# Kernel optimization log

Hardware: AMD Instinct MI355X
Metric: run time of the kernel (lower is better)

The kernel has to match this reference:

```python
import jax, jax.numpy as jnp
import numpy as np
import math

N, N_OBS, D, H, P = 500000, 200000, 32, 128, 4


def setup_inputs() -> dict:
    key = jax.random.key(0)
    ks = jax.random.split(key, 10)
    h = jax.random.normal(ks[0], (N, H), dtype=jnp.float32)
    p = jax.random.normal(ks[1], (N, 2 * D), dtype=jnp.float32)
    X_obs = jax.random.normal(ks[2], (N_OBS, D), dtype=jnp.float32)
    M_obs = (jax.random.uniform(ks[3], (N_OBS, D)) > 0.5).astype(jnp.float32)
    # unique sorted indices into [0, N) so the scatter-update is well defined
    i_obs = jnp.sort(jax.random.permutation(ks[4], N)[:N_OBS]).astype(jnp.int32)
    std = math.sqrt(2.0 / (4 + P))
    w_prep = std * jax.random.normal(ks[5], (D, 4, P), dtype=jnp.float32)
    bias_prep = 0.1 + jnp.zeros((D, P), dtype=jnp.float32)
    k = 1.0 / math.sqrt(H)
    W_ih = jax.random.uniform(ks[6], (3 * H, P * D), minval=-k, maxval=k, dtype=jnp.float32)
    W_hh = jax.random.uniform(ks[7], (3 * H, H), minval=-k, maxval=k, dtype=jnp.float32)
    b_ih = jax.random.uniform(ks[8], (3 * H,), minval=-k, maxval=k, dtype=jnp.float32)
    b_hh = jax.random.uniform(ks[9], (3 * H,), minval=-k, maxval=k, dtype=jnp.float32)
    return {"h": h, "p": p, "X_obs": X_obs, "M_obs": M_obs, "i_obs": i_obs,
            "w_prep": w_prep, "bias_prep": bias_prep,
            "W_ih": W_ih, "W_hh": W_hh, "b_ih": b_ih, "b_hh": b_hh}


def gru_cell(x, h, W_ih, W_hh, b_ih, b_hh):
    # torch.nn.GRUCell semantics; gate order r, z, n
    gi = x @ W_ih.T + b_ih            # [n, 3H]
    gh = h @ W_hh.T + b_hh            # [n, 3H]
    i_r, i_z, i_n = jnp.split(gi, 3, axis=1)
    h_r, h_z, h_n = jnp.split(gh, 3, axis=1)
    r = jax.nn.sigmoid(i_r + h_r)
    z = jax.nn.sigmoid(i_z + h_z)
    n = jnp.tanh(i_n + r * h_n)
    return (1.0 - z) * n + z * h


def reference(h, p, X_obs, M_obs, i_obs, w_prep, bias_prep, W_ih, W_hh, b_ih, b_hh):
    p_obs = p[i_obs]                                     # gather [n_obs, 2D]
    mean, logvar = jnp.split(p_obs, 2, axis=1)
    lv = jnp.clip(logvar, -10.0, 10.0)
    sigma = jnp.clip(jnp.exp(0.5 * lv), 1e-6, 1e6)
    error = jnp.clip((X_obs - mean) / sigma, -1e6, 1e6)
    log_lik_c = float(np.log(np.sqrt(2 * np.pi)))
    losses = 0.5 * ((error ** 2 + lv + 2.0 * log_lik_c) * M_obs)  # [n_obs, D]
    feats = jnp.stack([X_obs, mean, lv, error], axis=2)  # [n_obs, D, 4]
    gi = jnp.einsum('ndk,dkp->ndp', feats, w_prep) + bias_prep  # per-channel small matmul
    gi = jax.nn.relu(gi) * M_obs[..., None]              # mask broadcast over prep_hidden
    gru_in = gi.reshape(gi.shape[0], D * P)              # [n_obs, D*P], D-major like torch view
    h_obs = h[i_obs]
    h_new = gru_cell(gru_in, h_obs, W_ih, W_hh, b_ih, b_hh)
    h = h.at[i_obs].set(h_new)                           # scatter update
    return (h, losses)
```

## Files before the change

kernel.cpp:

```cpp
#include <hip/hip_runtime.h>


typedef __attribute__((ext_vector_type(8))) short bf16x8;
typedef __attribute__((ext_vector_type(4))) float f32x4;

__device__ inline unsigned short f2bf_rne(float x) {
    union { float f; unsigned int u; } v; v.f = x;
    unsigned int r = (v.u + 0x7fffu + ((v.u >> 16) & 1u)) >> 16;
    return (unsigned short)r;
}
__device__ inline unsigned short f2bf_tr(float x) {
    return (unsigned short)(__float_as_uint(x) >> 16);
}
__device__ inline float bf2f(unsigned short u) {
    return __uint_as_float(((unsigned int)u) << 16);
}
__device__ inline float fast_sigmoid(float x) {
    return __builtin_amdgcn_rcpf(1.f + __expf(-x));
}
__device__ inline float fast_tanh(float x) {
    const float a = fabsf(x);
    const float t = __expf(-2.f * a);
    const float r = (1.f - t) * __builtin_amdgcn_rcpf(1.f + t);
    return __builtin_copysignf(r, x);
}
__device__ inline void gl_lds16(const float* g, float* lds_base) {
    __builtin_amdgcn_global_load_lds(
        (const __attribute__((address_space(1))) void*)g,
        (__attribute__((address_space(3))) void*)lds_base, 16, 0, 0);
}

__global__ __launch_bounds__(256) void k_prepack(const float* __restrict__ W_ih,
                                                 const float* __restrict__ W_hh,
                                                 unsigned short* __restrict__ B) {
    const int i = blockIdx.x * 256 + threadIdx.x;
    const int w    = i / 12288;
    const int rem  = i - w * 12288;
    const int f    = rem >> 9;
    const int rem2 = rem & 511;
    const int l    = rem2 >> 3;
    const int j    = rem2 & 7;
    const int c    = w * 16 + (l & 15);
    const int ko   = (l >> 4) * 8 + j;
    float val;
    if (f < 8) {
        const int k = f * 32 + ko;
        val = (k < 128) ? W_ih[c * 128 + k] : W_hh[c * 128 + (k - 128)];
    } else if (f < 16) {
        const int k = (f - 8) * 32 + ko;
        val = (k < 128) ? W_ih[(128 + c) * 128 + k] : W_hh[(128 + c) * 128 + (k - 128)];
    } else if (f < 20) {
        const int k = (f - 16) * 32 + ko;
        val = W_ih[(256 + c) * 128 + k];
    } else {
        const int k = (f - 20 + 4) * 32 + ko;
        val = W_hh[(256 + c) * 128 + (k - 128)];
    }
    B[i] = f2bf_rne(val);
}

__global__ __launch_bounds__(256) void k_flag(const int* __restrict__ i_obs,
                                              unsigned char* __restrict__ flags, int n) {
    const int i = blockIdx.x * 256 + threadIdx.x;
    if (i < n) flags[i_obs[i]] = 1;
}

__global__ __launch_bounds__(256) void k_copy(const f32x4* __restrict__ src,
                                              f32x4* __restrict__ dst, long n4) {
    long i = (long)blockIdx.x * blockDim.x + threadIdx.x;
    long stride = (long)gridDim.x * blockDim.x;
    for (; i < n4; i += stride) dst[i] = src[i];
}

struct PrefRegs {
    float mean[4], lv[4], X[4], M[4];
    f32x4 hv[4];
    int idx[4];
};

__global__ __launch_bounds__(512) void k_pers(
    const float* __restrict__ h, const float* __restrict__ p,
    const float* __restrict__ X_obs, const float* __restrict__ M_obs,
    const int* __restrict__ i_obs,
    const float* __restrict__ w_prep, const float* __restrict__ bias_prep,
    const unsigned short* __restrict__ Bpk,
    const float* __restrict__ b_ih, const float* __restrict__ b_hh,
    float* __restrict__ out_h, float* __restrict__ out_losses,
    const unsigned char* __restrict__ flags,
    int NT, int chunk, int Nh, int do_copy)
{
    __shared__ unsigned short sA[4 * 8 * 64 * 8];
    __shared__ float hcopy[160 * 128];
    __shared__ int sIdx[64];

    const int tid  = threadIdx.x;
    const int d    = tid & 31;
    const int wid  = tid >> 6;
    const int lane = tid & 63;
    const int cw   = wid * 16 + (lane & 15);

    float wp[16], bp[4];
    #pragma unroll
    for (int t = 0; t < 16; ++t) wp[t] = w_prep[d * 16 + t];
    #pragma unroll
    for (int t = 0; t < 4; ++t) bp[t] = bias_prep[d * 4 + t];

    bf16x8 breg[24];
    {
        const bf16x8* bsrc = reinterpret_cast<const bf16x8*>(Bpk) + wid * 1536;
        #pragma unroll
        for (int f = 0; f < 24; ++f) breg[f] = bsrc[f * 64 + lane];
    }
    const float bR  = b_ih[cw]       + b_hh[cw];
    const float bZ  = b_ih[128 + cw] + b_hh[128 + cw];
    const float bIN = b_ih[256 + cw];
    const float bHN = b_hh[256 + cw];

    const int ksA  = d >> 3;
    const int l16  = ((d >> 1) & 3) * 16;
    const int j0   = (d & 1) * 4;
    const int ksE  = 4 + (cw >> 5);
    const int l16E = ((cw >> 3) & 3) * 16;
    const int jE   = cw & 7;

    const bf16x8* aptr = reinterpret_cast<const bf16x8*>(sA);

    PrefRegs R;

    auto G_load = [&](int t) {
        const int row0 = t * 64;
        #pragma unroll
        for (int ps = 0; ps < 4; ++ps) {
            const int r   = ps * 16 + (tid >> 5);
            const int idx = i_obs[row0 + r];
            R.idx[ps]  = idx;
            R.mean[ps] = p[(size_t)idx * 64 + d];
            R.lv[ps]   = p[(size_t)idx * 64 + 32 + d];
            R.X[ps]    = X_obs[(size_t)(row0 + r) * 32 + d];
            R.M[ps]    = M_obs[(size_t)(row0 + r) * 32 + d];
            R.hv[ps]   = *reinterpret_cast<const f32x4*>(h + (size_t)idx * 128 + d * 4);
        }
    };

    auto COPY_issue = [&](int t) {
        const long rlo = (long)t * chunk;
        const float* hs = h + rlo * 128;
        const int rbase = wid * 20;
        #pragma unroll
        for (int q = 0; q < 10; ++q) {
            const int row = rbase + q * 2;
            gl_lds16(hs + (size_t)row * 128 + lane * 4, &hcopy[row * 128]);
        }
    };

    auto COPY_store = [&](int t) {
        const long rlo = (long)t * chunk;
        f32x4* hd = reinterpret_cast<f32x4*>(out_h + rlo * 128);
        const unsigned char* fl = flags + rlo;
        const f32x4* hc = reinterpret_cast<const f32x4*>(hcopy);
        #pragma unroll
        for (int ii = 0; ii < 10; ++ii) {
            const int i5 = ii * 512 + tid;
            if (!fl[i5 >> 5]) __builtin_nontemporal_store(hc[i5], &hd[i5]);
        }
    };

    auto C_phase = [&](int t) {
        const int row0 = t * 64;
        #pragma unroll
        for (int ps = 0; ps < 4; ++ps) {
            const int r  = ps * 16 + (tid >> 5);
            const int mt = r >> 4;
            if (d == 0) sIdx[r] = R.idx[ps];
            const float lv      = fminf(fmaxf(R.lv[ps], -10.f), 10.f);
            const float inv_sig = __expf(-0.5f * lv);
            const float X = R.X[ps], Mv = R.M[ps], mean = R.mean[ps];
            const float err = fminf(fmaxf((X - mean) * inv_sig, -1e6f), 1e6f);
            out_losses[(size_t)(row0 + r) * 32 + d] =
                0.5f * ((err * err + lv + 1.8378770664093453f) * Mv);
            ushort4 u;
            float g0 = fmaf(X, wp[0], fmaf(mean, wp[4], fmaf(lv, wp[8],  fmaf(err, wp[12], bp[0]))));
            float g1 = fmaf(X, wp[1], fmaf(mean, wp[5], fmaf(lv, wp[9],  fmaf(err, wp[13], bp[1]))));
            float g2 = fmaf(X, wp[2], fmaf(mean, wp[6], fmaf(lv, wp[10], fmaf(err, wp[14], bp[2]))));
            float g3 = fmaf(X, wp[3], fmaf(mean, wp[7], fmaf(lv, wp[11], fmaf(err, wp[15], bp[3]))));
            u.x = f2bf_tr(fmaxf(g0, 0.f) * Mv);
            u.y = f2bf_tr(fmaxf(g1, 0.f) * Mv);
            u.z = f2bf_tr(fmaxf(g2, 0.f) * Mv);
            u.w = f2bf_tr(fmaxf(g3, 0.f) * Mv);
            *reinterpret_cast<ushort4*>(&sA[((mt * 8 + ksA) * 64 + (r & 15) + l16) * 8 + j0]) = u;
            const f32x4 v = R.hv[ps];
            ushort4 uh;
            uh.x = f2bf_tr(v.x); uh.y = f2bf_tr(v.y); uh.z = f2bf_tr(v.z); uh.w = f2bf_tr(v.w);
            *reinterpret_cast<ushort4*>(&sA[((mt * 8 + ksA + 4) * 64 + (r & 15) + l16) * 8 + j0]) = uh;
        }
    };

    auto M_phase = [&]() {
        #pragma unroll
        for (int mt = 0; mt < 4; ++mt) {
            f32x4 accR = {0.f, 0.f, 0.f, 0.f};
            f32x4 accZ = {0.f, 0.f, 0.f, 0.f};
            f32x4 accIN = {0.f, 0.f, 0.f, 0.f};
            f32x4 accHN = {0.f, 0.f, 0.f, 0.f};
            #pragma unroll
            for (int ks = 0; ks < 8; ++ks) {
                const bf16x8 af = aptr[(mt * 8 + ks) * 64 + lane];
                accR = __builtin_amdgcn_mfma_f32_16x16x32_bf16(af, breg[ks],     accR, 0, 0, 0);
                accZ = __builtin_amdgcn_mfma_f32_16x16x32_bf16(af, breg[8 + ks], accZ, 0, 0, 0);
                if (ks < 4) accIN = __builtin_amdgcn_mfma_f32_16x16x32_bf16(af, breg[16 + ks], accIN, 0, 0, 0);
                else        accHN = __builtin_amdgcn_mfma_f32_16x16x32_bf16(af, breg[16 + ks], accHN, 0, 0, 0);
            }
            const int r15b = (lane >> 4) * 4;
            #pragma unroll
            for (int reg = 0; reg < 4; ++reg) {
                const int r15 = r15b + reg;
                const int idx = sIdx[mt * 16 + r15];
                const float hp = bf2f(sA[((mt * 8 + ksE) * 64 + r15 + l16E) * 8 + jE]);
                const float xr  = accR[reg]  + bR;
                const float xz  = accZ[reg]  + bZ;
                const float xin = accIN[reg] + bIN;
                const float xhn = accHN[reg] + bHN;
                const float rg = fast_sigmoid(xr);
                const float zg = fast_sigmoid(xz);
                const float ng = fast_tanh(fmaf(rg, xhn, xin));
                out_h[(size_t)idx * 128 + cw] = fmaf(zg, hp - ng, ng);
            }
        }
    };

    int t = blockIdx.x;
    if (t >= NT) return;
    const int stride = gridDim.x;

    G_load(t);
    C_phase(t);
    __syncthreads();

    for (;;) {
        const int tn = t + stride;
        const bool has_next = (tn < NT);
        if (has_next) G_load(tn);
        if (do_copy) COPY_issue(t);
        M_phase();
        asm volatile("s_waitcnt vmcnt(16) lgkmcnt(0)" ::: "memory");
        __builtin_amdgcn_s_barrier();
        if (do_copy) COPY_store(t);
        if (!has_next) break;
        C_phase(tn);
        asm volatile("s_waitcnt lgkmcnt(0)" ::: "memory");
        __builtin_amdgcn_s_barrier();
        t = tn;
    }
}

extern "C" void kernel_launch(void* const* d_in, const int* in_sizes, int n_in,
                              void* d_out, int out_size, void* d_ws, size_t ws_size,
                              hipStream_t stream) {
    const float* h         = (const float*)d_in[0];
    const float* p         = (const float*)d_in[1];
    const float* X_obs     = (const float*)d_in[2];
    const float* M_obs     = (const float*)d_in[3];
    const int*   i_obs     = (const int*)d_in[4];
    const float* w_prep    = (const float*)d_in[5];
    const float* bias_prep = (const float*)d_in[6];
    const float* W_ih      = (const float*)d_in[7];
    const float* W_hh      = (const float*)d_in[8];
    const float* b_ih      = (const float*)d_in[9];
    const float* b_hh      = (const float*)d_in[10];

    const int Nh   = in_sizes[0] / 128;
    const int NOBS = in_sizes[4];
    const int NT   = NOBS / 64;
    const long n4  = (long)Nh * 128 / 4;

    float* out_h      = (float*)d_out;
    float* out_losses = out_h + (size_t)Nh * 128;

    unsigned short* Bpk   = (unsigned short*)d_ws;
    unsigned char*  flags = (unsigned char*)d_ws + (256 << 10);
    const size_t ws_needed = (256 << 10) + (size_t)Nh;

    hipLaunchKernelGGL(k_prepack, dim3(98304 / 256), dim3(256), 0, stream,
                       W_ih, W_hh, Bpk);

    const int chunk = (NT > 0) ? Nh / NT : 0;
    const int GRID  = 512;

    if (ws_size >= ws_needed && chunk == 160 && chunk * NT == Nh && NT * 64 == NOBS) {
        (void)hipMemsetAsync(flags, 0, (size_t)Nh, stream);
        hipLaunchKernelGGL(k_flag, dim3((NOBS + 255) / 256), dim3(256), 0, stream,
                           i_obs, flags, NOBS);
        hipLaunchKernelGGL(k_pers, dim3(GRID), dim3(512), 0, stream,
                           h, p, X_obs, M_obs, i_obs, w_prep, bias_prep, Bpk,
                           b_ih, b_hh, out_h, out_losses, flags, NT, chunk, Nh, 1);
    } else {
        hipLaunchKernelGGL(k_copy, dim3(4096), dim3(256), 0, stream,
                           (const f32x4*)h, (f32x4*)out_h, n4);
        hipLaunchKernelGGL(k_pers, dim3(GRID), dim3(512), 0, stream,
                           h, p, X_obs, M_obs, i_obs, w_prep, bias_prep, Bpk,
                           b_ih, b_hh, out_h, out_losses,
                           (const unsigned char*)nullptr, NT, chunk, Nh, 0);
    }
}
```

Baseline: 172.3 us.

## Double-buffer prefetch registers to load tiles two iterations ahead

The per-tile gather of indices, p, X, M and h rows now goes into two alternating register sets. Each set is loaded two tiles ahead of its compute phase, with the loop unrolled by two to swap buffers. The wait counts are adjusted so the copy loads complete while the extra gather loads stay in flight. This aims to hide global gather latency behind more work, at the cost of higher register pressure that may reduce occupancy or cause spills.

```diff
diff --git a/kernel.cpp b/kernel.cpp
--- a/kernel.cpp
+++ b/kernel.cpp
@@ -125,9 +125,9 @@
 
     const bf16x8* aptr = reinterpret_cast<const bf16x8*>(sA);
 
-    PrefRegs R;
-
-    auto G_load = [&](int t) {
+    PrefRegs RA, RB;
+
+    auto G_load = [&](int t, PrefRegs& R) {
         const int row0 = t * 64;
         #pragma unroll
         for (int ps = 0; ps < 4; ++ps) {
@@ -165,7 +165,7 @@
         }
     };
 
-    auto C_phase = [&](int t) {
+    auto C_phase = [&](int t, const PrefRegs& R) {
         const int row0 = t * 64;
         #pragma unroll
         for (int ps = 0; ps < 4; ++ps) {
@@ -228,29 +228,55 @@
         }
     };
 
+    #define BAR1(h2)                                                        \
+        if (h2) { asm volatile("s_waitcnt vmcnt(40) lgkmcnt(0)" ::: "memory"); } \
+        else    { asm volatile("s_waitcnt vmcnt(16) lgkmcnt(0)" ::: "memory"); } \
+        __builtin_amdgcn_s_barrier();
+    #define BAR2()                                                          \
+        asm volatile("s_waitcnt lgkmcnt(0)" ::: "memory");                  \
+        __builtin_amdgcn_s_barrier();
+
     int t = blockIdx.x;
     if (t >= NT) return;
     const int stride = gridDim.x;
 
-    G_load(t);
-    C_phase(t);
+    G_load(t, RA);
+    C_phase(t, RA);
+    int t1 = t + stride;
+    bool h1 = t1 < NT;
+    if (h1) G_load(t1, RB);
     __syncthreads();
 
     for (;;) {
-        const int tn = t + stride;
-        const bool has_next = (tn < NT);
-        if (has_next) G_load(tn);
-        if (do_copy) COPY_issue(t);
-        M_phase();
-        asm volatile("s_waitcnt vmcnt(16) lgkmcnt(0)" ::: "memory");
-        __builtin_amdgcn_s_barrier();
-        if (do_copy) COPY_store(t);
-        if (!has_next) break;
-        C_phase(tn);
-        asm volatile("s_waitcnt lgkmcnt(0)" ::: "memory");
-        __builtin_amdgcn_s_barrier();
-        t = tn;
+        {
+            const int t2 = t1 + stride;
+            const bool h2 = h1 && (t2 < NT);
+            if (do_copy) COPY_issue(t);
+            if (h2) G_load(t2, RA);
+            M_phase();
+            BAR1(h2);
+            if (do_copy) COPY_store(t);
+            if (!h1) break;
+            C_phase(t1, RB);
+            BAR2();
+            t = t1; t1 = t2; h1 = h2;
+        }
+        {
+            const int t2 = t1 + stride;
+            const bool h2 = h1 && (t2 < NT);
+            if (do_copy) COPY_issue(t);
+            if (h2) G_load(t2, RB);
+            M_phase();
+            BAR1(h2);
+            if (do_copy) COPY_store(t);
+            if (!h1) break;
+            C_phase(t1, RA);
+            BAR2();
+            t = t1; t1 = t2; h1 = h2;
+        }
     }
+    #undef BAR1
+    #undef BAR2
 }
 
 extern "C" void kernel_launch(void* const* d_in, const int* in_sizes, int n_in,
```

After: 264.8 us. +53.7%, slower.
